# Optimization experiments

Measured on AMD Instinct MI355X. Metric: run time of the kernel, lower is better.

## Reference

```python
import jax, jax.numpy as jnp
import numpy as np

B, S, D = 4, 4096, 1024


def setup_inputs() -> dict:
    key = jax.random.key(0)
    kx, kq, kk, kv = jax.random.split(key, 4)
    x = jax.random.normal(kx, (B, S, D), dtype=jnp.float32)
    W_q = jax.random.normal(kq, (D, D), dtype=jnp.float32) / np.sqrt(D)
    W_k = jax.random.normal(kk, (D, D), dtype=jnp.float32) / np.sqrt(D)
    W_v = jax.random.normal(kv, (D, D), dtype=jnp.float32) / np.sqrt(D)
    return {"x": x, "W_q": W_q, "W_k": W_k, "W_v": W_v}


def reference(x, W_q, W_k, W_v):
    # Projections: [B,S,D] @ [D,D] -> [B,S,D]
    Q = jnp.einsum('bsd,de->bse', x, W_q)
    K = jnp.einsum('bsd,de->bse', x, W_k)
    V = jnp.einsum('bsd,de->bse', x, W_v)
    scale = 1.0 / np.sqrt(D).astype(np.float32)
    # scores [B,S,S]; flash-attention computes softmax(QK^T/sqrt(d)) V exactly,
    # with rowmax/rowsum maintained in tiles -- mathematically identical to this.
    scores = jnp.einsum('bqd,bkd->bqk', Q, K) * scale
    probs = jax.nn.softmax(scores, axis=-1)
    out = jnp.einsum('bqk,bkd->bqd', probs, V)  # [B,S,D]
    return out
```

## Files before the change

kernel.cpp:

```cpp
#include <hip/hip_runtime.h>
#include <hip/hip_bf16.h>
#include <hip/hip_fp16.h>
#include <stdint.h>
#include <stddef.h>

typedef __attribute__((ext_vector_type(4))) float f32x4;
typedef __attribute__((ext_vector_type(8))) short s16x8;
typedef __attribute__((ext_vector_type(4))) short s16x4;

#define AS1 __attribute__((address_space(1)))
#define AS3 __attribute__((address_space(3)))

static __device__ __forceinline__ void gload_lds16(const void* g, void* l) {
  __builtin_amdgcn_global_load_lds((const AS1 void*)g, (AS3 void*)l, 16, 0, 0);
}

static __device__ __forceinline__ short bf16_bits(float f) {
  __hip_bfloat16 h = __float2bfloat16(f);
  union { __hip_bfloat16 h; short s; } u; u.h = h; return u.s;
}
static __device__ __forceinline__ short f16_bits(float f) {
  __half h = __float2half(f);
  union { __half h; short s; } u; u.h = h; return u.s;
}
static __device__ __forceinline__ float f16_to_f32(short b) {
  union { short s; __half h; } u; u.s = b; return __half2float(u.h);
}

template<int EPI>
__global__ __launch_bounds__(256, 2) void gemm_bt(
    const __hip_bfloat16* __restrict__ A,
    const __hip_bfloat16* __restrict__ Bt,
    void* __restrict__ Cv,
    int M, int N, int Kd,
    long zsA, long zsB, long zsC)
{
  __shared__ __hip_bfloat16 lds[2][2][128][32];
  A  += (long)blockIdx.z * zsA;
  Bt += (long)blockIdx.z * zsB;

  const int tid  = threadIdx.x;
  const int lane = tid & 63;
  const int wid  = tid >> 6;
  const int wm   = wid >> 1;
  const int wn   = wid & 1;
  const long bm  = (long)blockIdx.y * 128;
  const long bn  = (long)blockIdx.x * 128;

  const int lrow  = lane >> 2;
  const int pslot = lane & 3;

  f32x4 acc[4][4];
#pragma unroll
  for (int i = 0; i < 4; ++i)
#pragma unroll
    for (int j = 0; j < 4; ++j)
      acc[i][j] = (f32x4){0.f, 0.f, 0.f, 0.f};

  const int NK = Kd >> 5;

#define STAGE(buf, kt)                                                         \
  {                                                                            \
    _Pragma("unroll")                                                          \
    for (int half = 0; half < 2; ++half) {                                     \
      const int r  = wid * 32 + half * 16 + lrow;                              \
      const int ks = (pslot - ((r >> 1) & 3)) & 3;                             \
      const int kA = ((kt) << 5) + (ks << 3);                                  \
      gload_lds16(A  + (size_t)(bm + r) * Kd + kA,                             \
                  &lds[buf][0][wid * 32 + half * 16][0]);                      \
      gload_lds16(Bt + (size_t)(bn + r) * Kd + kA,                             \
                  &lds[buf][1][wid * 32 + half * 16][0]);                      \
    }                                                                          \
  }

  STAGE(0, 0);
  __syncthreads();

  for (int kt = 0; kt < NK; ++kt) {
    const int buf = kt & 1;
    if (kt + 1 < NK) STAGE(buf ^ 1, kt + 1);

    const int frow  = lane & 15;
    const int fslot = lane >> 4;
    s16x8 af[4], bfv[4];
#pragma unroll
    for (int mi = 0; mi < 4; ++mi) {
      const int r = wm * 64 + mi * 16 + frow;
      af[mi] = *(const s16x8*)&lds[buf][0][r][((fslot + (r >> 1)) & 3) << 3];
    }
#pragma unroll
    for (int ni = 0; ni < 4; ++ni) {
      const int r = wn * 64 + ni * 16 + frow;
      bfv[ni] = *(const s16x8*)&lds[buf][1][r][((fslot + (r >> 1)) & 3) << 3];
    }
#pragma unroll
    for (int mi = 0; mi < 4; ++mi)
#pragma unroll
      for (int ni = 0; ni < 4; ++ni)
        acc[mi][ni] = __builtin_amdgcn_mfma_f32_16x16x32_bf16(
            af[mi], bfv[ni], acc[mi][ni], 0, 0, 0);

    __syncthreads();
  }

  const int col   = lane & 15;
  const int rquad = (lane >> 4) << 2;
#pragma unroll
  for (int mi = 0; mi < 4; ++mi) {
#pragma unroll
    for (int ni = 0; ni < 4; ++ni) {
      const long m0 = bm + wm * 64 + mi * 16 + rquad;
      const long n  = bn + wn * 64 + ni * 16 + col;
#pragma unroll
      for (int j = 0; j < 4; ++j) {
        const float v = acc[mi][ni][j];
        if (EPI == 1) {
          float* C = (float*)Cv + (long)blockIdx.z * zsC;
          C[(size_t)(m0 + j) * N + n] = v;
        } else if (EPI == 4) {
          short* C = (short*)Cv + (long)blockIdx.z * zsC;
          C[(size_t)(m0 + j) * N + n] = f16_bits(v);
        } else {
          const int route = (int)(bn >> 10);
          __hip_bfloat16* base = (__hip_bfloat16*)Cv + (long)route * 16777216L;
          const long nl = n & 1023;
          const long m  = m0 + j;
          if (route < 2) {
            base[(size_t)m * 1024 + nl] = __float2bfloat16(v);
          } else {
            const long b = m >> 12;
            const long s = m & 4095;
            base[(((b << 10) + nl) << 12) + s] = __float2bfloat16(v);
          }
        }
      }
    }
  }
}

__global__ __launch_bounds__(256) void cvt_f32_bf16(
    const float* __restrict__ x, __hip_bfloat16* __restrict__ o, long n)
{
  const long i = ((long)blockIdx.x * 256 + threadIdx.x) * 8;
  if (i >= n) return;
  f32x4 a = *(const f32x4*)(x + i);
  f32x4 b = *(const f32x4*)(x + i + 4);
  s16x8 r;
  r[0] = bf16_bits(a.x); r[1] = bf16_bits(a.y);
  r[2] = bf16_bits(a.z); r[3] = bf16_bits(a.w);
  r[4] = bf16_bits(b.x); r[5] = bf16_bits(b.y);
  r[6] = bf16_bits(b.z); r[7] = bf16_bits(b.w);
  *(s16x8*)((short*)o + i) = r;
}

__global__ __launch_bounds__(256) void transpose_w_bf16(
    const float* __restrict__ W, __hip_bfloat16* __restrict__ Wt)
{
  __shared__ float t[32][33];
  const int tx = threadIdx.x & 31;
  const int ty = (threadIdx.x >> 5) * 4;
  const int bx = blockIdx.x * 32;
  const int by = blockIdx.y * 32;
#pragma unroll
  for (int j = 0; j < 4; ++j)
    t[ty + j][tx] = W[(size_t)(by + ty + j) * 1024 + bx + tx];
  __syncthreads();
#pragma unroll
  for (int j = 0; j < 4; ++j)
    Wt[(size_t)(bx + ty + j) * 1024 + by + tx] = __float2bfloat16(t[tx][ty + j]);
}

__global__ __launch_bounds__(256) void softmax_inplace(
    short* __restrict__ scP, float scale)
{
  __shared__ float red[4];
  const int t = threadIdx.x;
  short* pr = scP + (long)blockIdx.x * 4096;

  s16x8 h0 = *(const s16x8*)(pr + t * 8);
  s16x8 h1 = *(const s16x8*)(pr + 2048 + t * 8);
  float v[16];
  float mx = -3.4e38f;
#pragma unroll
  for (int j = 0; j < 8; ++j) { v[j]     = f16_to_f32(h0[j]); }
#pragma unroll
  for (int j = 0; j < 8; ++j) { v[8 + j] = f16_to_f32(h1[j]); }
#pragma unroll
  for (int i = 0; i < 16; ++i) mx = fmaxf(mx, v[i]);
#pragma unroll
  for (int off = 32; off >= 1; off >>= 1) mx = fmaxf(mx, __shfl_xor(mx, off));
  if ((t & 63) == 0) red[t >> 6] = mx;
  __syncthreads();
  mx = fmaxf(fmaxf(red[0], red[1]), fmaxf(red[2], red[3]));
  __syncthreads();

  float sum = 0.f;
#pragma unroll
  for (int i = 0; i < 16; ++i) { v[i] = __expf((v[i] - mx) * scale); sum += v[i]; }
#pragma unroll
  for (int off = 32; off >= 1; off >>= 1) sum += __shfl_xor(sum, off);
  if ((t & 63) == 0) red[t >> 6] = sum;
  __syncthreads();
  sum = red[0] + red[1] + red[2] + red[3];
  const float inv = 1.f / sum;

  s16x8 o0, o1;
#pragma unroll
  for (int j = 0; j < 8; ++j) { o0[j] = bf16_bits(v[j] * inv); }
#pragma unroll
  for (int j = 0; j < 8; ++j) { o1[j] = bf16_bits(v[8 + j] * inv); }
  *(s16x8*)(pr + t * 8) = o0;
  *(s16x8*)(pr + 2048 + t * 8) = o1;
}

extern "C" void kernel_launch(void* const* d_in, const int* in_sizes, int n_in,
                              void* d_out, int out_size, void* d_ws, size_t ws_size,
                              hipStream_t stream) {
  (void)in_sizes; (void)n_in; (void)out_size; (void)ws_size;
  const float* x  = (const float*)d_in[0];
  const float* Wq = (const float*)d_in[1];
  const float* Wk = (const float*)d_in[2];
  const float* Wv = (const float*)d_in[3];
  float* out = (float*)d_out;

  char* ws = (char*)d_ws;
  __hip_bfloat16* qb  = (__hip_bfloat16*)(ws);
  __hip_bfloat16* kb  = (__hip_bfloat16*)(ws + 33554432L);
  __hip_bfloat16* vt  = (__hip_bfloat16*)(ws + 67108864L);
  __hip_bfloat16* wt  = (__hip_bfloat16*)(ws + 100663296L);
  short*          scP = (short*)         (ws + 106954752L);
  __hip_bfloat16* xb  = (__hip_bfloat16*)(ws + 106954752L);

  cvt_f32_bf16<<<8192, 256, 0, stream>>>(x, xb, 16777216L);
  transpose_w_bf16<<<dim3(32, 32), 256, 0, stream>>>(Wq, wt);
  transpose_w_bf16<<<dim3(32, 32), 256, 0, stream>>>(Wk, wt + 1048576L);
  transpose_w_bf16<<<dim3(32, 32), 256, 0, stream>>>(Wv, wt + 2097152L);

  gemm_bt<3><<<dim3(24, 128, 1), 256, 0, stream>>>(
      xb, wt, qb, 16384, 3072, 1024, 0L, 0L, 0L);

  gemm_bt<4><<<dim3(32, 32, 4), 256, 0, stream>>>(
      qb, kb, scP, 4096, 4096, 1024,
      4194304L, 4194304L, 16777216L);

  softmax_inplace<<<16384, 256, 0, stream>>>(scP, 0.03125f);

  gemm_bt<1><<<dim3(8, 32, 4), 256, 0, stream>>>(
      (const __hip_bfloat16*)scP, vt, out, 4096, 1024, 4096,
      16777216L, 4194304L, 4194304L);
}
```

Before: 675.9 us.

## Grow GEMM tiles to 256x256 with 512 threads and triple-buffered LDS pipeline

The shared GEMM kernel now uses 256x256 output tiles computed by 8 wavefronts, each holding a 128x64 accumulator block. LDS goes from double to triple buffering, with loads issued two k-steps ahead and explicit vmcnt waits, split barriers and raised wave priority around the MFMA loop. The goal is more operand reuse per LDS byte and better hiding of global-load latency. The costs are more registers per thread (128 accumulator floats), 96KB of LDS per block, and fewer blocks in flight, which lowers occupancy and leaves a coarser grid for the smaller GEMMs.

```diff
diff --git a/kernel.cpp b/kernel.cpp
--- a/kernel.cpp
+++ b/kernel.cpp
@@ -27,39 +27,46 @@
   union { short s; __half h; } u; u.s = b; return __half2float(u.h);
 }
 
+#define WAITVM8   asm volatile("s_waitcnt vmcnt(8)" ::: "memory")
+#define WAITVM4   asm volatile("s_waitcnt vmcnt(4)" ::: "memory")
+#define WAITVM0   asm volatile("s_waitcnt vmcnt(0)" ::: "memory")
+#define WAITLGKM0 asm volatile("s_waitcnt lgkmcnt(0)" ::: "memory")
+#define SCHEDB    __builtin_amdgcn_sched_barrier(0)
+#define SBAR      __builtin_amdgcn_s_barrier()
+
 template<int EPI>
-__global__ __launch_bounds__(256, 2) void gemm_bt(
+__global__ __launch_bounds__(512, 2) void gemm256_bt(
     const __hip_bfloat16* __restrict__ A,
     const __hip_bfloat16* __restrict__ Bt,
     void* __restrict__ Cv,
     int M, int N, int Kd,
     long zsA, long zsB, long zsC)
 {
-  __shared__ __hip_bfloat16 lds[2][2][128][32];
+  __shared__ __hip_bfloat16 lds[3][2][256][32];
   A  += (long)blockIdx.z * zsA;
   Bt += (long)blockIdx.z * zsB;
 
   const int tid  = threadIdx.x;
   const int lane = tid & 63;
   const int wid  = tid >> 6;
-  const int wm   = wid >> 1;
-  const int wn   = wid & 1;
-  const long bm  = (long)blockIdx.y * 128;
-  const long bn  = (long)blockIdx.x * 128;
+  const int wm   = wid >> 2;
+  const int wn   = wid & 3;
+  const long bm  = (long)blockIdx.y * 256;
+  const long bn  = (long)blockIdx.x * 256;
 
   const int lrow  = lane >> 2;
   const int pslot = lane & 3;
 
-  f32x4 acc[4][4];
-#pragma unroll
-  for (int i = 0; i < 4; ++i)
+  f32x4 acc[8][4];
+#pragma unroll
+  for (int i = 0; i < 8; ++i)
 #pragma unroll
     for (int j = 0; j < 4; ++j)
       acc[i][j] = (f32x4){0.f, 0.f, 0.f, 0.f};
 
   const int NK = Kd >> 5;
 
-#define STAGE(buf, kt)                                                         \
+#define STAGE256(b, kt)                                                        \
   {                                                                            \
     _Pragma("unroll")                                                          \
     for (int half = 0; half < 2; ++half) {                                     \
@@ -67,49 +74,69 @@
       const int ks = (pslot - ((r >> 1) & 3)) & 3;                             \
       const int kA = ((kt) << 5) + (ks << 3);                                  \
       gload_lds16(A  + (size_t)(bm + r) * Kd + kA,                             \
-                  &lds[buf][0][wid * 32 + half * 16][0]);                      \
+                  &lds[b][0][wid * 32 + half * 16][0]);                        \
       gload_lds16(Bt + (size_t)(bn + r) * Kd + kA,                             \
-                  &lds[buf][1][wid * 32 + half * 16][0]);                      \
+                  &lds[b][1][wid * 32 + half * 16][0]);                        \
     }                                                                          \
   }
 
-  STAGE(0, 0);
-  __syncthreads();
-
-  for (int kt = 0; kt < NK; ++kt) {
-    const int buf = kt & 1;
-    if (kt + 1 < NK) STAGE(buf ^ 1, kt + 1);
-
-    const int frow  = lane & 15;
-    const int fslot = lane >> 4;
-    s16x8 af[4], bfv[4];
-#pragma unroll
-    for (int mi = 0; mi < 4; ++mi) {
-      const int r = wm * 64 + mi * 16 + frow;
-      af[mi] = *(const s16x8*)&lds[buf][0][r][((fslot + (r >> 1)) & 3) << 3];
-    }
+  STAGE256(0, 0);
+  if (NK > 1) STAGE256(1, 1);
+
+  int buf = 0;
+  int sb  = 2;
+
+  const int frow  = lane & 15;
+  const int fslot = lane >> 4;
+
+  for (int i = 0; i < NK; ++i) {
+    if (i + 2 < NK) {
+      STAGE256(sb, i + 2);
+      WAITVM8;
+    } else if (i + 2 == NK) {
+      WAITVM4;
+    } else {
+      WAITVM0;
+    }
+    SCHEDB;
+    SBAR;
+    SCHEDB;
+
+    s16x8 bfv[4];
 #pragma unroll
     for (int ni = 0; ni < 4; ++ni) {
       const int r = wn * 64 + ni * 16 + frow;
       bfv[ni] = *(const s16x8*)&lds[buf][1][r][((fslot + (r >> 1)) & 3) << 3];
     }
-#pragma unroll
-    for (int mi = 0; mi < 4; ++mi)
+    __builtin_amdgcn_s_setprio(1);
+#pragma unroll
+    for (int mi = 0; mi < 8; ++mi) {
+      const int r = wm * 128 + mi * 16 + frow;
+      const s16x8 af =
+          *(const s16x8*)&lds[buf][0][r][((fslot + (r >> 1)) & 3) << 3];
 #pragma unroll
       for (int ni = 0; ni < 4; ++ni)
         acc[mi][ni] = __builtin_amdgcn_mfma_f32_16x16x32_bf16(
-            af[mi], bfv[ni], acc[mi][ni], 0, 0, 0);
-
-    __syncthreads();
+            af, bfv[ni], acc[mi][ni], 0, 0, 0);
+    }
+    __builtin_amdgcn_s_setprio(0);
+
+    WAITLGKM0;
+    SCHEDB;
+    SBAR;
+    SCHEDB;
+
+    buf = (buf == 2) ? 0 : buf + 1;
+    sb  = (sb  == 2) ? 0 : sb  + 1;
   }
 
   const int col   = lane & 15;
   const int rquad = (lane >> 4) << 2;
 #pragma unroll
-  for (int mi = 0; mi < 4; ++mi) {
+  for (int mi = 0; mi < 8; ++mi) {
 #pragma unroll
     for (int ni = 0; ni < 4; ++ni) {
-      const long m0 = bm + wm * 64 + mi * 16 + rquad;
+      const long m0 = bm + wm * 128 + mi * 16 + rquad;
       const long n  = bn + wn * 64 + ni * 16 + col;
 #pragma unroll
       for (int j = 0; j < 4; ++j) {
@@ -236,16 +263,16 @@
   transpose_w_bf16<<<dim3(32, 32), 256, 0, stream>>>(Wk, wt + 1048576L);
   transpose_w_bf16<<<dim3(32, 32), 256, 0, stream>>>(Wv, wt + 2097152L);
 
-  gemm_bt<3><<<dim3(24, 128, 1), 256, 0, stream>>>(
+  gemm256_bt<3><<<dim3(12, 64, 1), 512, 0, stream>>>(
       xb, wt, qb, 16384, 3072, 1024, 0L, 0L, 0L);
 
-  gemm_bt<4><<<dim3(32, 32, 4), 256, 0, stream>>>(
+  gemm256_bt<4><<<dim3(16, 16, 4), 512, 0, stream>>>(
       qb, kb, scP, 4096, 4096, 1024,
       4194304L, 4194304L, 16777216L);
 
   softmax_inplace<<<16384, 256, 0, stream>>>(scP, 0.03125f);
 
-  gemm_bt<1><<<dim3(8, 32, 4), 256, 0, stream>>>(
+  gemm256_bt<1><<<dim3(4, 16, 4), 512, 0, stream>>>(
       (const __hip_bfloat16*)scP, vt, out, 4096, 1024, 4096,
       16777216L, 4194304L, 4194304L);
 }
```

After: 629.0 us. 1.07x faster.
